# Kernel optimization log

Measured on AMD Instinct MI355X. Metric: run time of the kernel, lower is better.

## Reference

```python
import jax, jax.numpy as jnp
import numpy as np

GCN_DEPTH = 2
PROP_ALPHA = 0.05
TANH_ALPHA = 3.0
SUBGRAPH = 20
SCALE_SET = (1.0, 0.8, 0.6, 0.5)
LAYERS = 3


def _tconv(x, W, b, stride):
    # x: (B,C,N,L), W: (O,I,1,k) -> VALID temporal conv along L
    y = jax.lax.conv_general_dilated(x, W, (1, stride), 'VALID',
                                     dimension_numbers=('NCHW', 'OIHW', 'NCHW'))
    return y + b[None, :, None, None]


def _build_adj(feat_scale, emb1, emb2, W1, b1, W2, b2, sfac):
    # dynamic graph: time-pooled scale features + static node embeddings
    feat = feat_scale.mean(axis=3).transpose(0, 2, 1)            # (B,N,C)
    n1 = jnp.tanh(TANH_ALPHA * sfac * (feat @ W1 + b1 + emb1))   # (B,N,D)
    n2 = jnp.tanh(TANH_ALPHA * sfac * (feat @ W2 + b2 + emb2))
    a = jnp.einsum('bnd,bmd->bnm', n1, n2) - jnp.einsum('bnd,bmd->bnm', n2, n1)
    adj = jax.nn.relu(jnp.tanh(TANH_ALPHA * a))                  # (B,N,N)
    kth = jax.lax.top_k(adj, SUBGRAPH)[0][..., -1:]              # per-row k-th value
    return adj * (adj >= kth).astype(adj.dtype)


def _mixprop(x, adj, W, b):
    # x: (B,C,N,L), adj: (B,N,N); gcn_depth-step alpha-mixed diffusion
    N = x.shape[2]
    A = adj + jnp.eye(N, dtype=adj.dtype)
    A = A / A.sum(axis=2, keepdims=True)
    h = x
    out = [h]
    for _ in range(GCN_DEPTH):
        h = PROP_ALPHA * x + (1.0 - PROP_ALPHA) * jnp.einsum('bcvl,bvw->bcwl', h, A)
        out.append(h)
    ho = jnp.concatenate(out, axis=1)                            # (B,(gdep+1)C,N,L)
    return jnp.einsum('bcnl,co->bonl', ho, W) + b[None, :, None, None]


def _forward(x, Ws, bs, scW0, scW1, scW2, scb, emb1, emb2,
             lin1W, lin1b, lin2W, lin2b, gW, gb,
             svW0, svW1, svW2, svb, s0W, s0b,
             gfW1, gfW2, e1W, e1b, e2W, e2b):
    # multi-scale block: 1x1 start conv then strided temporal convs
    h = jnp.einsum('bcnl,oc->bonl', x, Ws) + bs[None, :, None, None]
    scW = [scW0, scW1, scW2]
    scales = []
    for i in range(LAYERS):
        h = _tconv(h, scW[i], scb[i], 1 if i == 0 else 2)
        scales.append(h)
    # per-scale dynamic adjacency
    adjs = [_build_adj(scales[i], emb1, emb2, lin1W[i], lin1b[i],
                       lin2W[i], lin2b[i], SCALE_SET[i]) for i in range(LAYERS)]
    # scale0 head over raw input (dropout is identity in eval mode)
    out0 = jnp.einsum('bcnl,ocl->bon', x, s0W)[..., None] + s0b[None, :, None, None]
    outs = [out0]
    svW = [svW0, svW1, svW2]
    for i in range(LAYERS):
        g = (_mixprop(scales[i], adjs[i], gW[i, 0], gb[i, 0])
             + _mixprop(scales[i], adjs[i].transpose(0, 2, 1), gW[i, 1], gb[i, 1]))
        outs.append(jnp.einsum('bcnl,ocl->bon', g, svW[i])[..., None]
                    + svb[i][None, :, None, None])
    cat = jnp.concatenate(outs, axis=1)          # (B,(L+1)*Cs,N,1)
    stk = jnp.stack(outs, axis=1)                # (B,L+1,Cs,N,1)
    # SE-style gated fusion over scales
    se = cat.mean(axis=2)[..., 0]                # (B,(L+1)*Cs)
    se = jax.nn.sigmoid(jax.nn.relu(se @ gfW1) @ gfW2)   # (B,L+1)
    fused = (stk * se[:, :, None, None, None]).mean(axis=1)  # (B,Cs,N,1)
    y = jax.nn.relu(fused)
    y = jax.nn.relu(jnp.einsum('bcnl,oc->bonl', y, e1W) + e1b[None, :, None, None])
    y = jnp.einsum('bcnl,oc->bonl', y, e2W) + e2b[None, :, None, None]
    return y, jnp.stack(adjs)


def setup_inputs() -> dict:
    key = jax.random.key(0)
    ks = jax.random.split(key, 27)
    B, N, S, D = 4, 600, 168, 40
    Cc, Cs, Ce, Od = 32, 16, 128, 12
    L = [162, 79, 39]
    K = [7, 6, 3]
    r = lambda k, sh, s=0.1: jax.random.normal(k, sh, jnp.float32) * s
    return {
        'x': jax.random.normal(ks[0], (B, 1, N, S), jnp.float32),
        'Ws': r(ks[1], (Cc, 1)), 'bs': r(ks[2], (Cc,)),
        'scW0': r(ks[3], (Cc, Cc, 1, K[0])), 'scW1': r(ks[4], (Cc, Cc, 1, K[1])),
        'scW2': r(ks[5], (Cc, Cc, 1, K[2])), 'scb': r(ks[6], (3, Cc)),
        'emb1': r(ks[7], (N, D), 1.0), 'emb2': r(ks[8], (N, D), 1.0),
        'lin1W': r(ks[9], (3, Cc, D)), 'lin1b': r(ks[10], (3, D)),
        'lin2W': r(ks[11], (3, Cc, D)), 'lin2b': r(ks[12], (3, D)),
        'gW': r(ks[13], (3, 2, 3 * Cc, Cc)), 'gb': r(ks[14], (3, 2, Cc)),
        'svW0': r(ks[15], (Cs, Cc, L[0])), 'svW1': r(ks[16], (Cs, Cc, L[1])),
        'svW2': r(ks[17], (Cs, Cc, L[2])), 'svb': r(ks[18], (3, Cs)),
        's0W': r(ks[19], (Cs, 1, S)), 's0b': r(ks[20], (Cs,)),
        'gfW1': r(ks[21], (4 * Cs, 4)), 'gfW2': r(ks[22], (4, 4)),
        'e1W': r(ks[23], (Ce, Cs)), 'e1b': r(ks[24], (Ce,)),
        'e2W': r(ks[25], (Od, Ce)), 'e2b': r(ks[26], (Od,)),
    }


def reference(x, Ws, bs, scW0, scW1, scW2, scb, emb1, emb2,
              lin1W, lin1b, lin2W, lin2b, gW, gb,
              svW0, svW1, svW2, svb, s0W, s0b,
              gfW1, gfW2, e1W, e1b, e2W, e2b):
    return _forward(x, Ws, bs, scW0, scW1, scW2, scb, emb1, emb2,
                    lin1W, lin1b, lin2W, lin2b, gW, gb,
                    svW0, svW1, svW2, svb, s0W, s0b,
                    gfW1, gfW2, e1W, e1b, e2W, e2b)
```

## Files before the change

### kernel.cpp

```cpp
#include <hip/hip_runtime.h>
#include <math.h>


#define DW_WEFF 0
#define DW_CC   1536
#define DW_P    1632
#define DW_Q    9312
#define FB      19584
#define OW_CSV  (FB+0)
#define OW_CBIG (FB+48)
#define OW_VBIG (FB+304)
#define OW_T    (FB+760112)
#define OW_FEAT (FB+1374512)
#define OW_N1   (FB+1604912)
#define OW_N2   (FB+1892912)
#define OW_IRA  (FB+2180912)
#define OW_IRB  (FB+2188112)
#define OW_U1A  (FB+2195312)
#define OW_U2A  (FB+2310512)
#define OW_U1B  (FB+2425712)
#define OW_U2B  (FB+2540912)
#define OW_U3A  (FB+2656112)
#define OW_U3B  (FB+2771312)
#define OW_O    (FB+2886512)
#define OW_SE   (FB+3040112)

__device__ __forceinline__ float tanh_eigen(float x)
{
  const float CL = 7.99881172180175781f;
  float xc = fminf(fmaxf(x, -CL), CL);
  float x2 = __fmul_rn(xc, xc);
  float p = fmaf(x2, -2.76076847742355e-16f, 2.00018790482477e-13f);
  p = fmaf(x2, p, -8.60467152213735e-11f);
  p = fmaf(x2, p, 5.12229709037114e-08f);
  p = fmaf(x2, p, 1.48572235717979e-05f);
  p = fmaf(x2, p, 6.37261928875436e-04f);
  p = fmaf(x2, p, 4.89352455891786e-03f);
  p = __fmul_rn(xc, p);
  float q = fmaf(x2, 1.19825839466702e-06f, 1.18534705686654e-04f);
  q = fmaf(x2, q, 2.26843463243900e-03f);
  q = fmaf(x2, q, 4.89352518554385e-03f);
  float r = __fdiv_rn(p, q);
  return fabsf(x) < 0.0004f ? x : r;
}

__global__ __launch_bounds__(256) void k_pre_wc(const float* Ws, const float* bs,
    const float* scW0, const float* scW1, const float* scW2, const float* scb,
    const float* svW0, const float* svW1, const float* svW2,
    const float* gb, const float* svb, double* wd, float* ws)
{
  if (blockIdx.x < 48) {
    int blk = blockIdx.x;
    int i = blk/16, o = blk%16;
    const float* svW = (i==0)?svW0:((i==1)?svW1:svW2);
    int L = (i==0)?162:((i==1)?79:39);
    int tid = threadIdx.x;
    __shared__ double red[256];
    double s = 0;
    for (int idx = tid; idx < 32*L; idx += 256) {
      int o2 = idx / L, l = idx - o2*L;
      s += (double)svW[(o*32+o2)*L + l] * ((double)gb[(i*2+0)*32+o2] + (double)gb[(i*2+1)*32+o2]);
    }
    red[tid] = s; __syncthreads();
    for (int st = 128; st; st >>= 1) { if (tid < st) red[tid] += red[tid+st]; __syncthreads(); }
    if (tid == 0) ws[OW_CSV + blk] = (float)(red[0] + (double)svb[i*16+o]);
    return;
  }
  __shared__ double w0[32][7], c0[32], w1[32][12], c1[32];
  int t = threadIdx.x;
  for (int e = t; e < 32*7; e += 256) {
    int c = e/7, p = e%7; double s = 0;
    for (int ci = 0; ci < 32; ci++) s += (double)scW0[(c*32+ci)*7+p] * (double)Ws[ci];
    w0[c][p] = s;
  }
  for (int e = t; e < 32; e += 256) {
    double s = 0;
    for (int ci = 0; ci < 32; ci++) { double a = 0; for (int p = 0; p < 7; p++) a += (double)scW0[(e*32+ci)*7+p]; s += a*(double)bs[ci]; }
    c0[e] = s + (double)scb[e];
  }
  __syncthreads();
  for (int e = t; e < 32*12; e += 256) {
    int c = e/12, m = e%12; double s = 0;
    for (int k1 = 0; k1 < 6; k1++) { int k0 = m - k1; if (k0 < 0 || k0 > 6) continue;
      for (int ci = 0; ci < 32; ci++) s += (double)scW1[(c*32+ci)*6+k1] * w0[ci][k0]; }
    w1[c][m] = s;
  }
  for (int e = t; e < 32; e += 256) {
    double s = 0;
    for (int ci = 0; ci < 32; ci++) { double a = 0; for (int k1 = 0; k1 < 6; k1++) a += (double)scW1[(e*32+ci)*6+k1]; s += a*c0[ci]; }
    c1[e] = s + (double)scb[32+e];
  }
  __syncthreads();
  for (int e = t; e < 32*16; e += 256) {
    int c = e/16, p = e%16; double s = 0;
    for (int k2 = 0; k2 < 3; k2++) { int m = p - 2*k2; if (m < 0 || m > 11) continue;
      for (int ci = 0; ci < 32; ci++) s += (double)scW2[(c*32+ci)*3+k2] * w1[ci][m]; }
    wd[DW_WEFF + (2*32+c)*16 + p] = s;
  }
  for (int e = t; e < 32; e += 256) {
    double s = 0;
    for (int ci = 0; ci < 32; ci++) { double a = 0; for (int k2 = 0; k2 < 3; k2++) a += (double)scW2[(e*32+ci)*3+k2]; s += a*c1[ci]; }
    wd[DW_CC + 64 + e] = s + (double)scb[64+e];
  }
  for (int e = t; e < 32*7;  e += 256) wd[DW_WEFF + (e/7)*16  + e%7 ] = w0[e/7][e%7];
  for (int e = t; e < 32*12; e += 256) wd[DW_WEFF + (32 + e/12)*16 + e%12] = w1[e/12][e%12];
  for (int e = t; e < 32; e += 256) { wd[DW_CC+e] = c0[e]; wd[DW_CC+32+e] = c1[e]; }
}

__global__ __launch_bounds__(256) void k_pre_p(const float* gW, double* wd)
{
  int blk = blockIdx.x;
  int i = blk/5, g = blk%5;
  int tid = threadIdx.x;
  __shared__ float gls[2][3072];
  __shared__ double weffs[512];
  __shared__ double ccs[32];
  for (int e = tid; e < 6144; e += 256) gls[e >> 11 >= 1 ? (e/3072) : 0][e % 3072] = gW[i*6144 + e];
  for (int e = tid; e < 512; e += 256) weffs[e] = wd[DW_WEFF + i*512 + e];
  if (tid < 32) ccs[tid] = wd[DW_CC + i*32 + tid];
  __syncthreads();
  const float* g0 = gls[0];
  const float* g1 = gls[1];
  for (int e = tid; e < 512; e += 256) {
    int o2 = e >> 4, p = e & 15;
    double s = 0;
    for (int c = 0; c < 32; c++) {
      float w;
      if (g == 0) w = g0[c*32+o2] + g1[c*32+o2]
                    + 0.05f*(g0[(32+c)*32+o2] + g0[(64+c)*32+o2] + g1[(32+c)*32+o2] + g1[(64+c)*32+o2]);
      else if (g == 1) w = g0[(32+c)*32+o2];
      else if (g == 2) w = g0[(64+c)*32+o2];
      else if (g == 3) w = g1[(32+c)*32+o2];
      else             w = g1[(64+c)*32+o2];
      s += (double)w * weffs[c*16 + p];
    }
    wd[DW_P + ((i*5+g)*32 + o2)*16 + p] = s;
  }
  if (tid < 32) {
    int o2 = tid;
    double s = 0;
    for (int c = 0; c < 32; c++) {
      float w;
      if (g == 0) w = g0[c*32+o2] + g1[c*32+o2]
                    + 0.05f*(g0[(32+c)*32+o2] + g0[(64+c)*32+o2] + g1[(32+c)*32+o2] + g1[(64+c)*32+o2]);
      else if (g == 1) w = g0[(32+c)*32+o2];
      else if (g == 2) w = g0[(64+c)*32+o2];
      else if (g == 3) w = g1[(32+c)*32+o2];
      else             w = g1[(64+c)*32+o2];
      s += (double)w * ccs[c];
    }
    wd[DW_Q + (i*5+g)*32 + o2] = s;
  }
}

__global__ __launch_bounds__(256) void k_pre_v(const float* svW0, const float* svW1, const float* svW2,
                                               const float* s0W, const float* s0b, double* wd, float* ws)
{
  int jj = blockIdx.x;
  int tid = threadIdx.x;
  if (jj >= 240) {
    int o = jj - 240;
    if (tid < 168) ws[OW_VBIG + jj*168 + tid] = s0W[o*168 + tid];
    if (tid == 0)  ws[OW_CBIG + jj] = s0b[o];
    return;
  }
  int i = jj/80, g = (jj%80)/16, o = jj%16;
  int st = (i==0)?1:((i==1)?2:4), tp = (i==0)?7:((i==1)?12:16), L = (i==0)?162:((i==1)?79:39);
  const float* svW = (i==0)?svW0:((i==1)?svW1:svW2);
  const float* svo = svW + o*32*L;
  __shared__ float svlds[32*162];
  __shared__ double Pl[32][16];
  __shared__ double Qs[32];
  __shared__ double red[256];
  int NL = 32*L;
  for (int e = tid; e < NL; e += 256) svlds[e] = svo[e];
  for (int e = tid; e < 512; e += 256) {
    int o2 = e >> 4, p = e & 15;
    Pl[o2][p] = wd[DW_P + ((i*5+g)*32 + o2)*16 + p];
  }
  if (tid < 32) Qs[tid] = wd[DW_Q + (i*5+g)*32 + tid];
  __syncthreads();
  double s = 0;
  for (int e = tid; e < NL; e += 256) s += (double)svlds[e] * Qs[e / L];
  red[tid] = s; __syncthreads();
  for (int stp = 128; stp; stp >>= 1) { if (tid < stp) red[tid] += red[tid+stp]; __syncthreads(); }
  if (tid == 0) ws[OW_CBIG + jj] = (float)red[0];
  if (tid < 168) {
    int u = tid;
    int lo_ = u - tp + 1;
    int lmin = lo_ > 0 ? (lo_ + st - 1)/st : 0;
    int lmax = u/st; if (lmax > L-1) lmax = L-1;
    double v = 0.0;
    for (int o2 = 0; o2 < 32; o2++) {
      const float* sv = svlds + o2*L;
      const double* Pp = Pl[o2];
      for (int l = lmin; l <= lmax; l++)
        v += (double)sv[l] * Pp[u - st*l];
    }
    ws[OW_VBIG + jj*168 + u] = (float)v;
  }
}

__global__ __launch_bounds__(256) void k_fg(const float* x, double* wd, float* ws)
{
  int t = threadIdx.x;
  if (blockIdx.x >= 300) {
    __shared__ float xs[16][168];
    int r0 = (blockIdx.x - 300)*16;
    for (int e = t; e < 16*168; e += 256) { int r = e/168, u = e%168; xs[r][u] = x[(r0+r)*168 + u]; }
    __syncthreads();
    int jj = t;
    const float* V = ws + OW_VBIG + jj*168;
    double a[16];
    #pragma unroll
    for (int r = 0; r < 16; r++) a[r] = 0;
    for (int u = 0; u < 168; u++) {
      float wv = V[u];
      #pragma unroll
      for (int r = 0; r < 16; r++) a[r] += (double)wv * (double)xs[r][u];
    }
    double cb = (double)ws[OW_CBIG + jj];
    for (int r = 0; r < 16; r++)
      ws[OW_T + (r0+r)*256 + jj] = (float)(a[r] + cb);
    return;
  }
  int blk = blockIdx.x;
  int b = blk / 75, n0 = (blk % 75) * 8;
  __shared__ float xsf[8][168];
  __shared__ double xbar[8][35];
  for (int e = t; e < 8*168; e += 256) xsf[e/168][e%168] = x[(b*600 + n0 + e/168)*168 + e%168];
  __syncthreads();
  for (int e = t; e < 8*35; e += 256) {
    int nn = e/35, slot = e%35;
    int i = slot < 7 ? 0 : (slot < 19 ? 1 : 2);
    int p = slot - (i==0?0:(i==1?7:19));
    int st = (i==0)?1:((i==1)?2:4), L = (i==0)?162:((i==1)?79:39);
    double s = 0;
    for (int l = 0; l < L; l++) s += (double)xsf[nn][st*l+p];
    xbar[nn][slot] = s / (double)L;
  }
  __syncthreads();
  int nn = t >> 5, c = t & 31;
  for (int i = 0; i < 3; i++) {
    int off = (i==0)?0:((i==1)?7:19), tp = (i==0)?7:((i==1)?12:16);
    double f = wd[DW_CC + i*32 + c];
    for (int p = 0; p < tp; p++) f += wd[DW_WEFF + (i*32+c)*16 + p] * xbar[nn][off+p];
    ws[OW_FEAT + ((i*4+b)*600 + n0+nn)*32 + c] = (float)f;
  }
}

__global__ __launch_bounds__(256) void k_nodes(const float* lin1W, const float* lin1b,
                                               const float* lin2W, const float* lin2b,
                                               const float* emb1, const float* emb2, float* ws)
{
  int blk = blockIdx.x;
  int nt = blk % 38, b = (blk/38) % 4, i = blk/152;
  int n0 = nt*16;
  __shared__ float W1[1280], W2[1280], b1[40], b2[40], sf[16][33];
  int t = threadIdx.x;
  for (int e = t; e < 1280; e += 256) { W1[e] = lin1W[i*1280 + e]; W2[e] = lin2W[i*1280 + e]; }
  if (t < 40) { b1[t] = lin1b[i*40 + t]; b2[t] = lin2b[i*40 + t]; }
  for (int e = t; e < 16*32; e += 256) {
    int nn = e >> 5, c = e & 31; int n = n0 + nn;
    sf[nn][c] = (n < 600) ? ws[OW_FEAT + ((i*4+b)*600 + n)*32 + c] : 0.f;
  }
  __syncthreads();
  const float TSF[3] = {3.0f, 2.4f, 1.8f};
  for (int item = t; item < 16*80; item += 256) {
    int nn = item / 80, rr = item % 80;
    int n = n0 + nn; if (n >= 600) continue;
    int which = rr/40, d = rr%40;
    const float* W  = which ? W2 : W1;
    const float* bv = which ? b2 : b1;
    const float* em = which ? emb2 : emb1;
    float pre = 0.f;
    #pragma unroll
    for (int c = 0; c < 32; c++) pre = fmaf(sf[nn][c], W[c*40+d], pre);
    float p2 = __fadd_rn(pre, bv[d]);
    float p3 = __fadd_rn(p2, em[n*40+d]);
    float arg = __fmul_rn(TSF[i], p3);
    ws[(which ? OW_N2 : OW_N1) + ((i*4+b)*600 + n)*40 + d] = tanh_eigen(arg);
  }
}

__device__ __forceinline__ float4 adj_ld(const float* n1, const float* n2, int e, int w0)
{
  int mat = e >= 320; int idx = e - 320*mat;
  int jj = idx/10, q = idx - 10*jj;
  int w = w0 + jj;
  if (w < 600) return *(const float4*)((mat ? n2 : n1) + w*40 + 4*q);
  float4 z; z.x = z.y = z.z = z.w = 0.f; return z;
}

__global__ __launch_bounds__(256) void k_adj(float* adj_out, float* ws)
{
  int blk = blockIdx.x;
  int tile = blk % 75, b = (blk/75) % 4, i = blk/300;
  int row0 = tile*8;
  const float* n1 = ws + OW_N1 + (i*4+b)*24000;
  const float* n2 = ws + OW_N2 + (i*4+b)*24000;
  __shared__ float c1s[32][44], c2s[32][44];
  __shared__ float svals[8][604];
  int t = threadIdx.x;
  int rc = t & 7, jc = t >> 3;
  float am1[40], am2[40];
  {
    const float4* m1p = (const float4*)(n1 + (row0 + rc)*40);
    const float4* m2p = (const float4*)(n2 + (row0 + rc)*40);
    #pragma unroll
    for (int q = 0; q < 10; q++) {
      float4 v1 = m1p[q], v2 = m2p[q];
      am1[4*q]=v1.x; am1[4*q+1]=v1.y; am1[4*q+2]=v1.z; am1[4*q+3]=v1.w;
      am2[4*q]=v2.x; am2[4*q+1]=v2.y; am2[4*q+2]=v2.z; am2[4*q+3]=v2.w;
    }
  }
  float4 s0 = adj_ld(n1, n2, t, 0);
  float4 s1 = adj_ld(n1, n2, t + 256, 0);
  float4 s2; if (t < 128) s2 = adj_ld(n1, n2, t + 512, 0);
  for (int k = 0; k < 19; k++) {
    int w0 = 32*k;
    __syncthreads();
    {
      int e = t;       { int mat=e>=320, idx=e-320*mat, jj=idx/10, q=idx-10*jj, w=w0+jj;
                         if (w<600) *(float4*)(&(mat?c2s:c1s)[jj][4*q]) = s0; }
      e = t + 256;     { int mat=e>=320, idx=e-320*mat, jj=idx/10, q=idx-10*jj, w=w0+jj;
                         if (w<600) *(float4*)(&(mat?c2s:c1s)[jj][4*q]) = s1; }
      if (t < 128) { e = t + 512; int mat=e>=320, idx=e-320*mat, jj=idx/10, q=idx-10*jj, w=w0+jj;
                         if (w<600) *(float4*)(&(mat?c2s:c1s)[jj][4*q]) = s2; }
    }
    __syncthreads();
    if (k < 18) {
      int w0n = w0 + 32;
      s0 = adj_ld(n1, n2, t, w0n);
      s1 = adj_ld(n1, n2, t + 256, w0n);
      if (t < 128) s2 = adj_ld(n1, n2, t + 512, w0n);
    }
    if (jc < 32) {
      int w = w0 + jc;
      if (w < 600) {
        const float4* c2p = (const float4*)c2s[jc];
        const float4* c1p = (const float4*)c1s[jc];
        float d1 = 0.f, d2 = 0.f;
        #pragma unroll
        for (int q = 0; q < 10; q++) {
          float4 v = c2p[q];
          d1 = fmaf(am1[4*q], v.x, d1); d1 = fmaf(am1[4*q+1], v.y, d1);
          d1 = fmaf(am1[4*q+2], v.z, d1); d1 = fmaf(am1[4*q+3], v.w, d1);
        }
        #pragma unroll
        for (int q = 0; q < 10; q++) {
          float4 v = c1p[q];
          d2 = fmaf(am2[4*q], v.x, d2); d2 = fmaf(am2[4*q+1], v.y, d2);
          d2 = fmaf(am2[4*q+2], v.z, d2); d2 = fmaf(am2[4*q+3], v.w, d2);
        }
        float af = __fsub_rn(d1, d2);
        float tv = __fmul_rn(3.0f, af);
        float v = tanh_eigen(tv);
        svals[rc][w] = v > 0.f ? v : 0.f;
      }
    }
  }
  __syncthreads();
  int r = t >> 5, j = t & 31;
  float vv[19];
  #pragma unroll
  for (int k = 0; k < 19; k++) {
    int w = j + 32*k;
    vv[k] = (w < 600) ? svals[r][w] : 0.f;
  }
  float rm = 0.f;
  #pragma unroll
  for (int k = 0; k < 19; k++) rm = fmaxf(rm, vv[k]);
  #pragma unroll
  for (int s = 16; s; s >>= 1) rm = fmaxf(rm, __shfl_xor(rm, s, 32));
  const float VP = tanh_eigen(8.0f);
  unsigned int vpb = __float_as_uint(VP);
  int cntp = 0;
  #pragma unroll
  for (int k = 0; k < 19; k++) { int w = j + 32*k; if (w < 600 && __float_as_uint(vv[k]) >= vpb) cntp++; }
  #pragma unroll
  for (int s = 16; s; s >>= 1) cntp += __shfl_xor(cntp, s, 32);
  unsigned int lo, hi;
  unsigned int mb1 = __float_as_uint(rm) + 1u;
  if (cntp >= 20) { lo = vpb; hi = mb1; }
  else            { lo = 0u;  hi = vpb < mb1 ? vpb : mb1; }
  while (hi - lo > 1u) {
    unsigned int mid = lo + ((hi - lo) >> 1);
    int cnt = 0;
    #pragma unroll
    for (int k = 0; k < 19; k++) {
      int w = j + 32*k;
      if (w < 600 && __float_as_uint(vv[k]) >= mid) cnt++;
    }
    #pragma unroll
    for (int s = 16; s; s >>= 1) cnt += __shfl_xor(cnt, s, 32);
    if (cnt >= 20) lo = mid; else hi = mid;
  }
  unsigned int kb = lo;
  float* arow = adj_out + (i*4+b)*360000 + (row0+r)*600;
  float rsum = 0.f;
  #pragma unroll
  for (int k = 0; k < 19; k++) {
    int w = j + 32*k;
    if (w < 600) {
      float v = (__float_as_uint(vv[k]) >= kb) ? vv[k] : 0.f;
      arow[w] = v;
      rsum += v;
    }
  }
  #pragma unroll
  for (int s = 16; s; s >>= 1) rsum += __shfl_xor(rsum, s, 32);
  if (j == 0) ws[OW_IRA + (i*4+b)*600 + row0 + r] = 1.f/(1.f + rsum);
}

__global__ __launch_bounds__(256) void k_invrb(const float* adj, float* ws)
{
  int blk = blockIdx.x;
  int ib = blk / 10, wt = blk % 10;
  int tid = threadIdx.x;
  int wl = tid & 63, vg = tid >> 6;
  int w = wt*64 + wl;
  const float* A = adj + ib*360000;
  float s = 0.f;
  if (w < 600) {
    for (int v = vg*150; v < vg*150 + 150; v++) s += A[v*600 + w];
  }
  __shared__ float red[4][64];
  red[vg][wl] = s;
  __syncthreads();
  if (vg == 0 && w < 600) {
    float tot = ((red[0][wl] + red[1][wl]) + red[2][wl]) + red[3][wl];
    ws[OW_IRB + ib*600 + w] = 1.f/(1.f + tot);
  }
}

__global__ __launch_bounds__(256) void k_prop1(const float* adj, float* ws)
{
  int blk = blockIdx.x;
  int wt = blk % 19;
  int d  = (blk / 19) & 1;
  int ib = blk / 38;
  int i = ib >> 2, b = ib & 3;
  int w0 = wt * 32;
  const float* A   = adj + ib*360000;
  const float* irx = ws + (d ? OW_IRB : OW_IRA) + ib*600;
  const float* Tb  = ws + OW_T + (b*600)*256 + i*80 + 16 + d*32;
  __shared__ float As[4][32][36];
  __shared__ float Zs[4][32][36];
  __shared__ float red[3][64][17];
  int tid = threadIdx.x;
  int wv = tid >> 6, ln = tid & 63;
  int wq = ln >> 3, oq = ln & 7;
  float acc[4][4];
  #pragma unroll
  for (int a1 = 0; a1 < 4; a1++)
    #pragma unroll
    for (int a2 = 0; a2 < 4; a2++) acc[a1][a2] = 0.f;
  int vbeg = wv*160, vend = vbeg + 160 < 600 ? vbeg + 160 : 600;
  for (int v0 = vbeg; v0 < vend; v0 += 32) {
    if (d == 0) {
      #pragma unroll
      for (int q = 0; q < 4; q++) {
        int m = q*64 + ln, rr = m >> 3, c4 = (m & 7)*4;
        int v = v0 + rr;
        float4 av; av.x = av.y = av.z = av.w = 0.f;
        if (v < 600) {
          int wb = w0 + c4;
          if (wb + 3 < 600) av = *(const float4*)(A + v*600 + wb);
          else {
            if (wb+0 < 600) av.x = A[v*600 + wb+0];
            if (wb+1 < 600) av.y = A[v*600 + wb+1];
            if (wb+2 < 600) av.z = A[v*600 + wb+2];
            if (wb+3 < 600) av.w = A[v*600 + wb+3];
          }
        }
        *(float4*)(&As[wv][rr][c4]) = av;
      }
    } else {
      #pragma unroll
      for (int q = 0; q < 4; q++) {
        int m = q*64 + ln, rr = m >> 3, c4 = (m & 7)*4;
        int w = w0 + rr;
        float4 av; av.x = av.y = av.z = av.w = 0.f;
        if (w < 600) {
          if (v0 + c4 + 3 < 600) av = *(const float4*)(A + w*600 + v0 + c4);
          else {
            if (v0+c4+0 < 600) av.x = A[w*600 + v0+c4+0];
            if (v0+c4+1 < 600) av.y = A[w*600 + v0+c4+1];
            if (v0+c4+2 < 600) av.z = A[w*600 + v0+c4+2];
            if (v0+c4+3 < 600) av.w = A[w*600 + v0+c4+3];
          }
        }
        As[wv][c4+0][rr] = av.x; As[wv][c4+1][rr] = av.y;
        As[wv][c4+2][rr] = av.z; As[wv][c4+3][rr] = av.w;
      }
    }
    #pragma unroll
    for (int q = 0; q < 4; q++) {
      int m = q*64 + ln, rr = m >> 3, c4 = (m & 7)*4;
      int v = v0 + rr;
      float4 zv; zv.x = zv.y = zv.z = zv.w = 0.f;
      if (v < 600) {
        float ir = irx[v];
        float4 tv = *(const float4*)(Tb + v*256 + c4);
        zv.x = ir*tv.x; zv.y = ir*tv.y; zv.z = ir*tv.z; zv.w = ir*tv.w;
      }
      *(float4*)(&Zs[wv][rr][c4]) = zv;
    }
    __builtin_amdgcn_s_waitcnt(0);
    for (int vl = 0; vl < 32; vl++) {
      float4 a4 = *(const float4*)(&As[wv][vl][wq*4]);
      float4 z4 = *(const float4*)(&Zs[wv][vl][oq*4]);
      acc[0][0] = fmaf(a4.x, z4.x, acc[0][0]); acc[0][1] = fmaf(a4.x, z4.y, acc[0][1]);
      acc[0][2] = fmaf(a4.x, z4.z, acc[0][2]); acc[0][3] = fmaf(a4.x, z4.w, acc[0][3]);
      acc[1][0] = fmaf(a4.y, z4.x, acc[1][0]); acc[1][1] = fmaf(a4.y, z4.y, acc[1][1]);
      acc[1][2] = fmaf(a4.y, z4.z, acc[1][2]); acc[1][3] = fmaf(a4.y, z4.w, acc[1][3]);
      acc[2][0] = fmaf(a4.z, z4.x, acc[2][0]); acc[2][1] = fmaf(a4.z, z4.y, acc[2][1]);
      acc[2][2] = fmaf(a4.z, z4.z, acc[2][2]); acc[2][3] = fmaf(a4.z, z4.w, acc[2][3]);
      acc[3][0] = fmaf(a4.w, z4.x, acc[3][0]); acc[3][1] = fmaf(a4.w, z4.y, acc[3][1]);
      acc[3][2] = fmaf(a4.w, z4.z, acc[3][2]); acc[3][3] = fmaf(a4.w, z4.w, acc[3][3]);
    }
  }
  if (wv > 0) {
    #pragma unroll
    for (int kw = 0; kw < 4; kw++)
      #pragma unroll
      for (int ko = 0; ko < 4; ko++) red[wv-1][ln][kw*4+ko] = acc[kw][ko];
  }
  __syncthreads();
  if (wv == 0) {
    #pragma unroll
    for (int kw = 0; kw < 4; kw++) {
      int w = w0 + wq*4 + kw;
      if (w >= 600) continue;
      float irw = irx[w];
      #pragma unroll
      for (int ko = 0; ko < 4; ko++) {
        int oz = oq*4 + ko;
        float sum = acc[kw][ko] + red[0][ln][kw*4+ko] + red[1][ln][kw*4+ko] + red[2][ln][kw*4+ko];
        sum += irw * Tb[w*256 + oz];
        float* dst = ws + (d==0 ? (oz < 16 ? OW_U1A : OW_U2A) : (oz < 16 ? OW_U1B : OW_U2B));
        dst[(ib*600 + w)*16 + (oz & 15)] = sum;
      }
    }
  }
}

__global__ __launch_bounds__(256) void k_prop2(const float* adj, float* ws)
{
  int blk = blockIdx.x;
  int wt = blk % 19;
  int d  = (blk / 19) & 1;
  int ib = blk / 38;
  int w0 = wt * 32;
  const float* A   = adj + ib*360000;
  const float* irx = ws + (d ? OW_IRB : OW_IRA) + ib*600;
  const float* u2x = ws + (d ? OW_U2B : OW_U2A) + ib*9600;
  __shared__ float As[4][32][36];
  __shared__ float Zs[4][32][20];
  __shared__ float red[3][64][9];
  int tid = threadIdx.x;
  int wv = tid >> 6, ln = tid & 63;
  int wq = ln >> 3, oq = ln & 7;
  float acc[4][2];
  #pragma unroll
  for (int a1 = 0; a1 < 4; a1++) { acc[a1][0] = 0.f; acc[a1][1] = 0.f; }
  int vbeg = wv*160, vend = vbeg + 160 < 600 ? vbeg + 160 : 600;
  for (int v0 = vbeg; v0 < vend; v0 += 32) {
    if (d == 0) {
      #pragma unroll
      for (int q = 0; q < 4; q++) {
        int m = q*64 + ln, rr = m >> 3, c4 = (m & 7)*4;
        int v = v0 + rr;
        float4 av; av.x = av.y = av.z = av.w = 0.f;
        if (v < 600) {
          int wb = w0 + c4;
          if (wb + 3 < 600) av = *(const float4*)(A + v*600 + wb);
          else {
            if (wb+0 < 600) av.x = A[v*600 + wb+0];
            if (wb+1 < 600) av.y = A[v*600 + wb+1];
            if (wb+2 < 600) av.z = A[v*600 + wb+2];
            if (wb+3 < 600) av.w = A[v*600 + wb+3];
          }
        }
        *(float4*)(&As[wv][rr][c4]) = av;
      }
    } else {
      #pragma unroll
      for (int q = 0; q < 4; q++) {
        int m = q*64 + ln, rr = m >> 3, c4 = (m & 7)*4;
        int w = w0 + rr;
        float4 av; av.x = av.y = av.z = av.w = 0.f;
        if (w < 600) {
          if (v0 + c4 + 3 < 600) av = *(const float4*)(A + w*600 + v0 + c4);
          else {
            if (v0+c4+0 < 600) av.x = A[w*600 + v0+c4+0];
            if (v0+c4+1 < 600) av.y = A[w*600 + v0+c4+1];
            if (v0+c4+2 < 600) av.z = A[w*600 + v0+c4+2];
            if (v0+c4+3 < 600) av.w = A[w*600 + v0+c4+3];
          }
        }
        As[wv][c4+0][rr] = av.x; As[wv][c4+1][rr] = av.y;
        As[wv][c4+2][rr] = av.z; As[wv][c4+3][rr] = av.w;
      }
    }
    #pragma unroll
    for (int q = 0; q < 2; q++) {
      int m = q*64 + ln, rr = m >> 2, c4 = (m & 3)*4;
      int v = v0 + rr;
      float4 zv; zv.x = zv.y = zv.z = zv.w = 0.f;
      if (v < 600) {
        float ir = irx[v];
        float4 uv = *(const float4*)(u2x + v*16 + c4);
        zv.x = ir*uv.x; zv.y = ir*uv.y; zv.z = ir*uv.z; zv.w = ir*uv.w;
      }
      *(float4*)(&Zs[wv][rr][c4]) = zv;
    }
    __builtin_amdgcn_s_waitcnt(0);
    for (int vl = 0; vl < 32; vl++) {
      float4 a4 = *(const float4*)(&As[wv][vl][wq*4]);
      float2 z2 = *(const float2*)(&Zs[wv][vl][oq*2]);
      acc[0][0] = fmaf(a4.x, z2.x, acc[0][0]); acc[0][1] = fmaf(a4.x, z2.y, acc[0][1]);
      acc[1][0] = fmaf(a4.y, z2.x, acc[1][0]); acc[1][1] = fmaf(a4.y, z2.y, acc[1][1]);
      acc[2][0] = fmaf(a4.z, z2.x, acc[2][0]); acc[2][1] = fmaf(a4.z, z2.y, acc[2][1]);
      acc[3][0] = fmaf(a4.w, z2.x, acc[3][0]); acc[3][1] = fmaf(a4.w, z2.y, acc[3][1]);
    }
  }
  if (wv > 0) {
    #pragma unroll
    for (int kw = 0; kw < 4; kw++) {
      red[wv-1][ln][kw*2+0] = acc[kw][0];
      red[wv-1][ln][kw*2+1] = acc[kw][1];
    }
  }
  __syncthreads();
  if (wv == 0) {
    float* dst = ws + (d==0 ? OW_U3A : OW_U3B);
    #pragma unroll
    for (int kw = 0; kw < 4; kw++) {
      int w = w0 + wq*4 + kw;
      if (w >= 600) continue;
      float irw = irx[w];
      #pragma unroll
      for (int ko = 0; ko < 2; ko++) {
        int oz = oq*2 + ko;
        float sum = acc[kw][ko] + red[0][ln][kw*2+ko] + red[1][ln][kw*2+ko] + red[2][ln][kw*2+ko];
        sum += irw * u2x[w*16 + oz];
        dst[(ib*600 + w)*16 + oz] = sum;
      }
    }
  }
}

__global__ void k_outs(float* ws)
{
  int e = blockIdx.x*256 + threadIdx.x;
  if (e >= 153600) return;
  int n = e % 600, o = (e/600) % 16, b = (e/9600) % 4, s = e/38400;
  float val;
  if (s == 0) {
    val = ws[OW_T + (b*600+n)*256 + 240 + o];
  } else {
    int i = s - 1;
    int idx = ((i*4+b)*600 + n)*16 + o;
    float t0 = ws[OW_T + (b*600+n)*256 + i*80 + o];
    val = t0 + 0.95f  * (ws[OW_U1A+idx] + ws[OW_U1B+idx])
             + 0.0475f* (ws[OW_U2A+idx] + ws[OW_U2B+idx])
             + 0.9025f* (ws[OW_U3A+idx] + ws[OW_U3B+idx])
             + ws[OW_CSV + i*16 + o];
  }
  ws[OW_O + ((s*4+b)*16 + o)*600 + n] = val;
}

__global__ void k_se(const float* gfW1, const float* gfW2, float* ws)
{
  __shared__ float sv[4][64], hb[4][4];
  int t = threadIdx.x, b = t >> 6, k = t & 63;
  const float* Op = ws + OW_O + (((k>>4)*4 + b)*16 + (k & 15))*600;
  float s = 0.f;
  for (int n = 0; n < 600; n++) s += Op[n];
  sv[b][k] = s * (1.f/600.f);
  __syncthreads();
  if (t < 16) {
    int bb = t >> 2, j = t & 3;
    float h = 0.f;
    for (int kk = 0; kk < 64; kk++) h += sv[bb][kk]*gfW1[kk*4+j];
    hb[bb][j] = h > 0.f ? h : 0.f;
  }
  __syncthreads();
  if (t < 16) {
    int bb = t >> 2, ii = t & 3;
    float g = 0.f;
    for (int j = 0; j < 4; j++) g += hb[bb][j]*gfW2[j*4+ii];
    ws[OW_SE + bb*4 + ii] = 1.f/(1.f + expf(-g));
  }
}

__global__ __launch_bounds__(128) void k_head(const float* e1W, const float* e1b,
                                              const float* e2W, const float* e2b,
                                              float* ws, float* dout)
{
  int blk = blockIdx.x, b = blk/600, n = blk%600;
  __shared__ float y0[16], y1[128];
  int t = threadIdx.x;
  if (t < 16) {
    float f = 0.f;
    for (int s = 0; s < 4; s++) f += ws[OW_SE + b*4 + s] * ws[OW_O + ((s*4+b)*16 + t)*600 + n];
    f *= 0.25f;
    y0[t] = f > 0.f ? f : 0.f;
  }
  __syncthreads();
  {
    float h = e1b[t];
    for (int o = 0; o < 16; o++) h += e1W[t*16+o]*y0[o];
    y1[t] = h > 0.f ? h : 0.f;
  }
  __syncthreads();
  if (t < 96) {
    int o = t >> 3, part = t & 7;
    float v = 0.f;
    #pragma unroll
    for (int e = 0; e < 16; e++) v = fmaf(e2W[o*128 + part*16 + e], y1[part*16 + e], v);
    #pragma unroll
    for (int s = 4; s; s >>= 1) v += __shfl_down(v, s, 8);
    if (part == 0) dout[b*7200 + o*600 + n] = e2b[o] + v;
  }
}

extern "C" void kernel_launch(void* const* d_in, const int* in_sizes, int n_in,
                              void* d_out, int out_size, void* d_ws, size_t ws_size,
                              hipStream_t stream)
{
  const float* x    = (const float*)d_in[0];
  const float* Ws   = (const float*)d_in[1];
  const float* bs   = (const float*)d_in[2];
  const float* scW0 = (const float*)d_in[3];
  const float* scW1 = (const float*)d_in[4];
  const float* scW2 = (const float*)d_in[5];
  const float* scb  = (const float*)d_in[6];
  const float* emb1 = (const float*)d_in[7];
  const float* emb2 = (const float*)d_in[8];
  const float* lin1W= (const float*)d_in[9];
  const float* lin1b= (const float*)d_in[10];
  const float* lin2W= (const float*)d_in[11];
  const float* lin2b= (const float*)d_in[12];
  const float* gW   = (const float*)d_in[13];
  const float* gb   = (const float*)d_in[14];
  const float* svW0 = (const float*)d_in[15];
  const float* svW1 = (const float*)d_in[16];
  const float* svW2 = (const float*)d_in[17];
  const float* svb  = (const float*)d_in[18];
  const float* s0W  = (const float*)d_in[19];
  const float* s0b  = (const float*)d_in[20];
  const float* gfW1 = (const float*)d_in[21];
  const float* gfW2 = (const float*)d_in[22];
  const float* e1W  = (const float*)d_in[23];
  const float* e1b  = (const float*)d_in[24];
  const float* e2W  = (const float*)d_in[25];
  const float* e2b  = (const float*)d_in[26];
  float* out = (float*)d_out;
  float* ws  = (float*)d_ws;
  double* wd = (double*)d_ws;
  float* adj_out = out + 28800;

  k_pre_wc<<<49, 256, 0, stream>>>(Ws, bs, scW0, scW1, scW2, scb,
                                   svW0, svW1, svW2, gb, svb, wd, ws);
  k_pre_p<<<15, 256, 0, stream>>>(gW, wd);
  k_pre_v<<<256, 256, 0, stream>>>(svW0, svW1, svW2, s0W, s0b, wd, ws);
  k_fg<<<450, 256, 0, stream>>>(x, wd, ws);
  k_nodes<<<456, 256, 0, stream>>>(lin1W, lin1b, lin2W, lin2b, emb1, emb2, ws);
  k_adj<<<900, 256, 0, stream>>>(adj_out, ws);
  k_invrb<<<120, 256, 0, stream>>>(adj_out, ws);
  k_prop1<<<456, 256, 0, stream>>>(adj_out, ws);
  k_prop2<<<456, 256, 0, stream>>>(adj_out, ws);
  k_outs<<<600, 256, 0, stream>>>(ws);
  k_se<<<1, 256, 0, stream>>>(gfW1, gfW2, ws);
  k_head<<<2400, 128, 0, stream>>>(e1W, e1b, e2W, e2b, ws, out);
}
```

Before: 252.5 us.

## Double-buffer adjacency tiles and fuse SE mean reduction into output kernel

k_adj now keeps two shared-memory buffers for the n1/n2 column tiles. Each iteration writes the next tile while computing on the current one, which drops one of the two barriers per iteration. k_outs now reduces each output row with warp shuffles and atomics into a new workspace area, so k_se no longer reads all 600 columns serially with a single block. This adds a memset launch, float atomics that make the summation order nondeterministic, and more LDS use in k_adj.

```diff
diff --git a/kernel.cpp b/kernel.cpp
--- a/kernel.cpp
+++ b/kernel.cpp
@@ -24,6 +24,7 @@
 #define OW_U3B  (FB+2771312)
 #define OW_O    (FB+2886512)
 #define OW_SE   (FB+3040112)
+#define OW_SVS  (FB+3040128)
 
 __device__ __forceinline__ float tanh_eigen(float x)
 {
@@ -115,7 +116,7 @@
   __shared__ float gls[2][3072];
   __shared__ double weffs[512];
   __shared__ double ccs[32];
-  for (int e = tid; e < 6144; e += 256) gls[e >> 11 >= 1 ? (e/3072) : 0][e % 3072] = gW[i*6144 + e];
+  for (int e = tid; e < 6144; e += 256) gls[e/3072][e % 3072] = gW[i*6144 + e];
   for (int e = tid; e < 512; e += 256) weffs[e] = wd[DW_WEFF + i*512 + e];
   if (tid < 32) ccs[tid] = wd[DW_CC + i*32 + tid];
   __syncthreads();
@@ -299,7 +300,7 @@
   int row0 = tile*8;
   const float* n1 = ws + OW_N1 + (i*4+b)*24000;
   const float* n2 = ws + OW_N2 + (i*4+b)*24000;
-  __shared__ float c1s[32][44], c2s[32][44];
+  __shared__ float c1s[2][32][44], c2s[2][32][44];
   __shared__ float svals[8][604];
   int t = threadIdx.x;
   int rc = t & 7, jc = t >> 3;
@@ -314,32 +315,38 @@
       am2[4*q]=v2.x; am2[4*q+1]=v2.y; am2[4*q+2]=v2.z; am2[4*q+3]=v2.w;
     }
   }
-  float4 s0 = adj_ld(n1, n2, t, 0);
-  float4 s1 = adj_ld(n1, n2, t + 256, 0);
-  float4 s2; if (t < 128) s2 = adj_ld(n1, n2, t + 512, 0);
+  int e0 = t,       m0 = e0 >= 320, i0 = e0 - 320*m0, j0 = i0/10, q0 = i0 - 10*j0;
+  int e1 = t + 256, m1_ = e1 >= 320, i1 = e1 - 320*m1_, j1 = i1/10, q1 = i1 - 10*j1;
+  int e2 = t + 512, m2_ = 1,        i2 = e2 - 320,     j2 = i2/10, q2 = i2 - 10*j2;
+  float4 s0, s1, s2;
+  s0 = adj_ld(n1, n2, t, 0); s1 = adj_ld(n1, n2, t + 256, 0); if (t < 128) s2 = adj_ld(n1, n2, t + 512, 0);
+  { int w;
+    w = 0 + j0; if (w < 600) *(float4*)(&(m0 ? c2s : c1s)[0][j0][4*q0]) = s0;
+    w = 0 + j1; if (w < 600) *(float4*)(&(m1_ ? c2s : c1s)[0][j1][4*q1]) = s1;
+    if (t < 128) { w = 0 + j2; if (w < 600) *(float4*)(&c2s[0][j2][4*q2]) = s2; }
+  }
+  s0 = adj_ld(n1, n2, t, 32); s1 = adj_ld(n1, n2, t + 256, 32); if (t < 128) s2 = adj_ld(n1, n2, t + 512, 32);
+  __syncthreads();
   for (int k = 0; k < 19; k++) {
+    int cur = k & 1;
     int w0 = 32*k;
-    __syncthreads();
+    if (k < 18) {
+      int w0n = w0 + 32; int w;
+      w = w0n + j0; if (w < 600) *(float4*)(&(m0 ? c2s : c1s)[cur^1][j0][4*q0]) = s0;
+      w = w0n + j1; if (w < 600) *(float4*)(&(m1_ ? c2s : c1s)[cur^1][j1][4*q1]) = s1;
+      if (t < 128) { w = w0n + j2; if (w < 600) *(float4*)(&c2s[cur^1][j2][4*q2]) = s2; }
+      if (k < 17) {
+        int w0nn = w0 + 64;
+        s0 = adj_ld(n1, n2, t, w0nn);
+        s1 = adj_ld(n1, n2, t + 256, w0nn);
+        if (t < 128) s2 = adj_ld(n1, n2, t + 512, w0nn);
+      }
+    }
     {
-      int e = t;       { int mat=e>=320, idx=e-320*mat, jj=idx/10, q=idx-10*jj, w=w0+jj;
-                         if (w<600) *(float4*)(&(mat?c2s:c1s)[jj][4*q]) = s0; }
-      e = t + 256;     { int mat=e>=320, idx=e-320*mat, jj=idx/10, q=idx-10*jj, w=w0+jj;
-                         if (w<600) *(float4*)(&(mat?c2s:c1s)[jj][4*q]) = s1; }
-      if (t < 128) { e = t + 512; int mat=e>=320, idx=e-320*mat, jj=idx/10, q=idx-10*jj, w=w0+jj;
-                         if (w<600) *(float4*)(&(mat?c2s:c1s)[jj][4*q]) = s2; }
-    }
-    __syncthreads();
-    if (k < 18) {
-      int w0n = w0 + 32;
-      s0 = adj_ld(n1, n2, t, w0n);
-      s1 = adj_ld(n1, n2, t + 256, w0n);
-      if (t < 128) s2 = adj_ld(n1, n2, t + 512, w0n);
-    }
-    if (jc < 32) {
       int w = w0 + jc;
       if (w < 600) {
-        const float4* c2p = (const float4*)c2s[jc];
-        const float4* c1p = (const float4*)c1s[jc];
+        const float4* c2p = (const float4*)c2s[cur][jc];
+        const float4* c1p = (const float4*)c1s[cur][jc];
         float d1 = 0.f, d2 = 0.f;
         #pragma unroll
         for (int q = 0; q < 10; q++) {
@@ -359,8 +366,8 @@
         svals[rc][w] = v > 0.f ? v : 0.f;
       }
     }
-  }
-  __syncthreads();
+    __syncthreads();
+  }
   int r = t >> 5, j = t & 31;
   float vv[19];
   #pragma unroll
@@ -652,34 +659,56 @@
   }
 }
 
-__global__ void k_outs(float* ws)
-{
-  int e = blockIdx.x*256 + threadIdx.x;
-  if (e >= 153600) return;
-  int n = e % 600, o = (e/600) % 16, b = (e/9600) % 4, s = e/38400;
-  float val;
-  if (s == 0) {
-    val = ws[OW_T + (b*600+n)*256 + 240 + o];
-  } else {
-    int i = s - 1;
-    int idx = ((i*4+b)*600 + n)*16 + o;
-    float t0 = ws[OW_T + (b*600+n)*256 + i*80 + o];
-    val = t0 + 0.95f  * (ws[OW_U1A+idx] + ws[OW_U1B+idx])
-             + 0.0475f* (ws[OW_U2A+idx] + ws[OW_U2B+idx])
-             + 0.9025f* (ws[OW_U3A+idx] + ws[OW_U3B+idx])
-             + ws[OW_CSV + i*16 + o];
-  }
-  ws[OW_O + ((s*4+b)*16 + o)*600 + n] = val;
+__global__ __launch_bounds__(256) void k_outs(float* ws)
+{
+  __shared__ float sums[2];
+  int tid = threadIdx.x;
+  int e = blockIdx.x*256 + tid;
+  int rA = (blockIdx.x*256)/600;
+  if (tid < 2) sums[tid] = 0.f;
+  __syncthreads();
+  float val = 0.f;
+  int row = rA;
+  if (e < 153600) {
+    int n = e % 600, o = (e/600) % 16, b = (e/9600) % 4, s = e/38400;
+    if (s == 0) {
+      val = ws[OW_T + (b*600+n)*256 + 240 + o];
+    } else {
+      int i = s - 1;
+      int idx = ((i*4+b)*600 + n)*16 + o;
+      float t0 = ws[OW_T + (b*600+n)*256 + i*80 + o];
+      val = t0 + 0.95f  * (ws[OW_U1A+idx] + ws[OW_U1B+idx])
+               + 0.0475f* (ws[OW_U2A+idx] + ws[OW_U2B+idx])
+               + 0.9025f* (ws[OW_U3A+idx] + ws[OW_U3B+idx])
+               + ws[OW_CSV + i*16 + o];
+    }
+    ws[OW_O + ((s*4+b)*16 + o)*600 + n] = val;
+    row = e/600;
+  }
+  float vA = (e < 153600 && row == rA) ? val : 0.f;
+  float vB = (e < 153600 && row == rA+1) ? val : 0.f;
+  #pragma unroll
+  for (int s = 32; s; s >>= 1) { vA += __shfl_down(vA, s, 64); vB += __shfl_down(vB, s, 64); }
+  if ((tid & 63) == 0) {
+    if (vA != 0.f) atomicAdd(&sums[0], vA);
+    if (vB != 0.f) atomicAdd(&sums[1], vB);
+  }
+  __syncthreads();
+  if (tid < 2) {
+    int r = rA + tid;
+    if (r < 256) atomicAdd(&ws[OW_SVS + r], sums[tid]);
+  }
 }
 
 __global__ void k_se(const float* gfW1, const float* gfW2, float* ws)
 {
   __shared__ float sv[4][64], hb[4][4];
-  int t = threadIdx.x, b = t >> 6, k = t & 63;
-  const float* Op = ws + OW_O + (((k>>4)*4 + b)*16 + (k & 15))*600;
-  float s = 0.f;
-  for (int n = 0; n < 600; n++) s += Op[n];
-  sv[b][k] = s * (1.f/600.f);
+  int t = threadIdx.x;
+  {
+    int row = t;
+    int o = row & 15, b = (row >> 4) & 3, s = row >> 6;
+    sv[b][s*16 + o] = ws[OW_SVS + row] * (1.f/600.f);
+  }
   __syncthreads();
   if (t < 16) {
     int bb = t >> 2, j = t & 3;
@@ -773,6 +802,7 @@
   k_invrb<<<120, 256, 0, stream>>>(adj_out, ws);
   k_prop1<<<456, 256, 0, stream>>>(adj_out, ws);
   k_prop2<<<456, 256, 0, stream>>>(adj_out, ws);
+  hipMemsetAsync((void*)(ws + OW_SVS), 0, 256*sizeof(float), stream);
   k_outs<<<600, 256, 0, stream>>>(ws);
   k_se<<<1, 256, 0, stream>>>(gfW1, gfW2, ws);
   k_head<<<2400, 128, 0, stream>>>(e1W, e1b, e2W, e2b, ws, out);
```

Result: faster. 236.4 us (-6.3%).

## Fuse column sums into adjacency kernel and row sums into output kernel

Applied to the files above, without the earlier changes.

The adjacency kernel now keeps each block's masked rows in shared memory and atomically accumulates per-column sums. This replaces the separate k_invrb pass that re-read the full adjacency matrix from global memory. k_outs also reduces its outputs per row with wave shuffles and atomics, so k_se no longer loops over 600 elements per channel. The cost is a memset, extra atomics, and float summation order that is no longer deterministic.

```diff
diff --git a/kernel.cpp b/kernel.cpp
--- a/kernel.cpp
+++ b/kernel.cpp
@@ -24,6 +24,8 @@
 #define OW_U3B  (FB+2771312)
 #define OW_O    (FB+2886512)
 #define OW_SE   (FB+3040112)
+#define OW_SVS  (FB+3040128)
+#define OW_CSB  (FB+3040384)
 
 __device__ __forceinline__ float tanh_eigen(float x)
 {
@@ -115,7 +117,7 @@
   __shared__ float gls[2][3072];
   __shared__ double weffs[512];
   __shared__ double ccs[32];
-  for (int e = tid; e < 6144; e += 256) gls[e >> 11 >= 1 ? (e/3072) : 0][e % 3072] = gW[i*6144 + e];
+  for (int e = tid; e < 6144; e += 256) gls[e/3072][e % 3072] = gW[i*6144 + e];
   for (int e = tid; e < 512; e += 256) weffs[e] = wd[DW_WEFF + i*512 + e];
   if (tid < 32) ccs[tid] = wd[DW_CC + i*32 + tid];
   __syncthreads();
@@ -405,33 +407,29 @@
     if (w < 600) {
       float v = (__float_as_uint(vv[k]) >= kb) ? vv[k] : 0.f;
       arow[w] = v;
+      svals[r][w] = v;
       rsum += v;
     }
   }
   #pragma unroll
   for (int s = 16; s; s >>= 1) rsum += __shfl_xor(rsum, s, 32);
   if (j == 0) ws[OW_IRA + (i*4+b)*600 + row0 + r] = 1.f/(1.f + rsum);
-}
-
-__global__ __launch_bounds__(256) void k_invrb(const float* adj, float* ws)
-{
-  int blk = blockIdx.x;
-  int ib = blk / 10, wt = blk % 10;
-  int tid = threadIdx.x;
-  int wl = tid & 63, vg = tid >> 6;
-  int w = wt*64 + wl;
-  const float* A = adj + ib*360000;
-  float s = 0.f;
-  if (w < 600) {
-    for (int v = vg*150; v < vg*150 + 150; v++) s += A[v*600 + w];
-  }
-  __shared__ float red[4][64];
-  red[vg][wl] = s;
-  __syncthreads();
-  if (vg == 0 && w < 600) {
-    float tot = ((red[0][wl] + red[1][wl]) + red[2][wl]) + red[3][wl];
-    ws[OW_IRB + ib*600 + w] = 1.f/(1.f + tot);
-  }
+  __syncthreads();
+  {
+    float* csb = ws + OW_CSB + (i*4+b)*600;
+    for (int w = t; w < 600; w += 256) {
+      float cs = 0.f;
+      #pragma unroll
+      for (int rr2 = 0; rr2 < 8; rr2++) cs += svals[rr2][w];
+      atomicAdd(&csb[w], cs);
+    }
+  }
+}
+
+__global__ void k_invrb(float* ws)
+{
+  int e = blockIdx.x*256 + threadIdx.x;
+  if (e < 7200) ws[OW_IRB + e] = 1.f/(1.f + ws[OW_CSB + e]);
 }
 
 __global__ __launch_bounds__(256) void k_prop1(const float* adj, float* ws)
@@ -652,34 +650,56 @@
   }
 }
 
-__global__ void k_outs(float* ws)
-{
-  int e = blockIdx.x*256 + threadIdx.x;
-  if (e >= 153600) return;
-  int n = e % 600, o = (e/600) % 16, b = (e/9600) % 4, s = e/38400;
-  float val;
-  if (s == 0) {
-    val = ws[OW_T + (b*600+n)*256 + 240 + o];
-  } else {
-    int i = s - 1;
-    int idx = ((i*4+b)*600 + n)*16 + o;
-    float t0 = ws[OW_T + (b*600+n)*256 + i*80 + o];
-    val = t0 + 0.95f  * (ws[OW_U1A+idx] + ws[OW_U1B+idx])
-             + 0.0475f* (ws[OW_U2A+idx] + ws[OW_U2B+idx])
-             + 0.9025f* (ws[OW_U3A+idx] + ws[OW_U3B+idx])
-             + ws[OW_CSV + i*16 + o];
-  }
-  ws[OW_O + ((s*4+b)*16 + o)*600 + n] = val;
+__global__ __launch_bounds__(256) void k_outs(float* ws)
+{
+  __shared__ float sums[2];
+  int tid = threadIdx.x;
+  int e = blockIdx.x*256 + tid;
+  int rA = (blockIdx.x*256)/600;
+  if (tid < 2) sums[tid] = 0.f;
+  __syncthreads();
+  float val = 0.f;
+  int row = rA;
+  if (e < 153600) {
+    int n = e % 600, o = (e/600) % 16, b = (e/9600) % 4, s = e/38400;
+    if (s == 0) {
+      val = ws[OW_T + (b*600+n)*256 + 240 + o];
+    } else {
+      int i = s - 1;
+      int idx = ((i*4+b)*600 + n)*16 + o;
+      float t0 = ws[OW_T + (b*600+n)*256 + i*80 + o];
+      val = t0 + 0.95f  * (ws[OW_U1A+idx] + ws[OW_U1B+idx])
+               + 0.0475f* (ws[OW_U2A+idx] + ws[OW_U2B+idx])
+               + 0.9025f* (ws[OW_U3A+idx] + ws[OW_U3B+idx])
+               + ws[OW_CSV + i*16 + o];
+    }
+    ws[OW_O + ((s*4+b)*16 + o)*600 + n] = val;
+    row = e/600;
+  }
+  float vA = (e < 153600 && row == rA) ? val : 0.f;
+  float vB = (e < 153600 && row == rA+1) ? val : 0.f;
+  #pragma unroll
+  for (int s = 32; s; s >>= 1) { vA += __shfl_down(vA, s, 64); vB += __shfl_down(vB, s, 64); }
+  if ((tid & 63) == 0) {
+    if (vA != 0.f) atomicAdd(&sums[0], vA);
+    if (vB != 0.f) atomicAdd(&sums[1], vB);
+  }
+  __syncthreads();
+  if (tid < 2) {
+    int r = rA + tid;
+    if (r < 256) atomicAdd(&ws[OW_SVS + r], sums[tid]);
+  }
 }
 
 __global__ void k_se(const float* gfW1, const float* gfW2, float* ws)
 {
   __shared__ float sv[4][64], hb[4][4];
-  int t = threadIdx.x, b = t >> 6, k = t & 63;
-  const float* Op = ws + OW_O + (((k>>4)*4 + b)*16 + (k & 15))*600;
-  float s = 0.f;
-  for (int n = 0; n < 600; n++) s += Op[n];
-  sv[b][k] = s * (1.f/600.f);
+  int t = threadIdx.x;
+  {
+    int row = t;
+    int o = row & 15, b = (row >> 4) & 3, s = row >> 6;
+    sv[b][s*16 + o] = ws[OW_SVS + row] * (1.f/600.f);
+  }
   __syncthreads();
   if (t < 16) {
     int bb = t >> 2, j = t & 3;
@@ -767,10 +787,11 @@
                                    svW0, svW1, svW2, gb, svb, wd, ws);
   k_pre_p<<<15, 256, 0, stream>>>(gW, wd);
   k_pre_v<<<256, 256, 0, stream>>>(svW0, svW1, svW2, s0W, s0b, wd, ws);
+  hipMemsetAsync((void*)(ws + OW_SVS), 0, (256 + 7200)*sizeof(float), stream);
   k_fg<<<450, 256, 0, stream>>>(x, wd, ws);
   k_nodes<<<456, 256, 0, stream>>>(lin1W, lin1b, lin2W, lin2b, emb1, emb2, ws);
   k_adj<<<900, 256, 0, stream>>>(adj_out, ws);
-  k_invrb<<<120, 256, 0, stream>>>(adj_out, ws);
+  k_invrb<<<29, 256, 0, stream>>>(ws);
   k_prop1<<<456, 256, 0, stream>>>(adj_out, ws);
   k_prop2<<<456, 256, 0, stream>>>(adj_out, ws);
   k_outs<<<600, 256, 0, stream>>>(ws);
```

After: 234.9 us (median of 2 runs). 7.0% less time.
